# Kernel tuning notes

Hardware: AMD Instinct MI355X
Metric: run time of the kernel (lower is better)

## Reference

```python
import jax, jax.numpy as jnp
import numpy as np

N_NODES = 100000
N_EDGES = 1600000
MAX_RADIUS = 3.0
NUM_BASIS = 3
SQRT2 = 2.0 ** 0.5
# e3nn soft_one_hot_linspace 'smooth_finite' prefactor
C_SMOOTH = 1.14136 * float(np.exp(2.0))


def _sus(x):
    # smooth unit step: exp(-1/x) for x>0 else 0 (NaN-safe for grad)
    safe = jnp.where(x > 0.0, x, 1.0)
    return jnp.where(x > 0.0, jnp.exp(-1.0 / safe), 0.0)


def radial_embed(d):
    # soft_one_hot_linspace(d, 0, max_radius, 3, basis='smooth_finite', cutoff=True) * sqrt(num_basis)
    values = jnp.linspace(0.0, MAX_RADIUS, NUM_BASIS + 2)[1:-1]  # [3]
    step = MAX_RADIUS / (NUM_BASIS + 1)
    diff = (d[:, None] - values) / step  # [E,3]
    y = C_SMOOTH * _sus(diff + 1.0) * _sus(1.0 - diff)
    return y * (NUM_BASIS ** 0.5)


def fcnet(x, w1, w2):
    # e3nn FullyConnectedNet([3,16,numel], relu): normalized weights, normalize2mom(relu)=sqrt(2)*relu
    h = SQRT2 * jax.nn.relu(x @ (w1 / w1.shape[0] ** 0.5))
    return h @ (w2 / w2.shape[0] ** 0.5)


def reference(pos, feat, edge_src, edge_dst, fc1_w1, fc1_w2, core_w1, core_w2, fc3_w1, fc3_w2, conv_w, conv_b):
    n = pos.shape[0]
    z = edge_src.shape[0] / n  # average num neighbors
    edge_vec = pos[edge_dst] - pos[edge_src]
    d = jnp.sqrt(jnp.sum(edge_vec * edge_vec, axis=1))  # edges are self-loop-free -> d > 0
    emb = radial_embed(d)  # [E,3]

    # NOTE on e3nn math: with input/mid/output parities all even and sh = 0e+1o+2e,
    # the only parity-allowed paths producing nonzero output are the 0e (scalar) paths,
    # which contract against Y_0 = 1 ('component' normalization). The 4x1e block of the
    # mid irreps is identically zero (no parity-allowed path ever populates it), so the
    # math below (scalar block only, with e3nn path weights) is exactly equivalent.
    def conv(x, w1, w2, mul_in, mul_out, path_w):
        # per-edge weights from radial MLP; keep the 0e->0e instruction block
        w = fcnet(emb, w1, w2)[:, : mul_in * mul_out].reshape(-1, mul_in, mul_out)
        msg = path_w * jnp.einsum('euw,eu->ew', w, x[edge_src])
        return jax.ops.segment_sum(msg, edge_dst, num_segments=n) / z ** 0.5

    x = conv(feat, fc1_w1, fc1_w2, 3, 4, (1.0 / 3.0) ** 0.5)  # tp1: fan_in 3*1 -> pw=1/sqrt(3)
    for i in range(3):
        x = conv(x, core_w1[i], core_w2[i], 4, 4, 0.5)  # tp2 0e path: pw=sqrt(1/4)
    x = conv(x, fc3_w1, fc3_w2, 4, 16, 0.5)  # tp3: pw=sqrt(1/4)
    # Conv1d(16, 2, 1) == pointwise linear
    return x @ conv_w.T + conv_b


def setup_inputs():
    key = jax.random.key(0)
    ks = jax.random.split(key, 12)
    pos = jax.random.uniform(ks[0], (N_NODES, 3), dtype=jnp.float32)  # unit box -> all edge lengths < max_radius
    feat = jax.random.normal(ks[1], (N_NODES, 3), dtype=jnp.float32)
    edge_src = jax.random.randint(ks[2], (N_EDGES,), 0, N_NODES, dtype=jnp.int32)
    off = jax.random.randint(ks[3], (N_EDGES,), 1, N_NODES, dtype=jnp.int32)
    edge_dst = ((edge_src + off) % N_NODES).astype(jnp.int32)  # radius_graph has no self-loops
    return {
        'pos': pos,
        'feat': feat,
        'edge_src': edge_src,
        'edge_dst': edge_dst,
        'fc1_w1': jax.random.normal(ks[4], (3, 16), jnp.float32),
        'fc1_w2': jax.random.normal(ks[5], (16, 12), jnp.float32),
        'core_w1': jax.random.normal(ks[6], (3, 3, 16), jnp.float32),
        'core_w2': jax.random.normal(ks[7], (3, 16, 48), jnp.float32),
        'fc3_w1': jax.random.normal(ks[8], (3, 16), jnp.float32),
        'fc3_w2': jax.random.normal(ks[9], (16, 64), jnp.float32),
        'conv_w': jax.random.normal(ks[10], (2, 16), jnp.float32) * 0.25,
        'conv_b': jax.random.normal(ks[11], (2,), jnp.float32) * 0.1,
    }
```

## Files before the change

kernel.cpp:

```cpp
#include <hip/hip_runtime.h>


#define BCAP 4608
#define NBMAX 400

__device__ __forceinline__ float sus_f(float x) {
    return x > 0.0f ? __expf(-1.0f / x) : 0.0f;
}

__device__ __forceinline__ float uload(const float* p) {
    return __uint_as_float(__builtin_amdgcn_readfirstlane(__float_as_uint(*p)));
}

__global__ __launch_bounds__(256) void k_bin(
    const int* __restrict__ src, const int* __restrict__ dst,
    int* __restrict__ gcur, int* __restrict__ ebuf_int,
    int nedges, int nb)
{
    __shared__ int cnt[NBMAX];
    __shared__ int gb[NBMAX];
    for (int b = threadIdx.x; b < nb; b += 256) cnt[b] = 0;
    __syncthreads();
    int base = blockIdx.x * 2048;
    int pk[8]; int bk[8]; short r[8];
    #pragma unroll
    for (int i = 0; i < 8; ++i) {
        int e = base + i * 256 + threadIdx.x;
        if (e < nedges) {
            int s = src[e], t = dst[e];
            int b = t >> 8;
            bk[i] = b;
            pk[i] = (s << 8) | (t & 255);
            r[i] = (short)atomicAdd(&cnt[b], 1);
        } else bk[i] = -1;
    }
    __syncthreads();
    for (int b = threadIdx.x; b < nb; b += 256) {
        int c = cnt[b];
        gb[b] = c > 0 ? atomicAdd(&gcur[b], c) : 0;
    }
    __syncthreads();
    #pragma unroll
    for (int i = 0; i < 8; ++i) {
        if (bk[i] >= 0) {
            int p = gb[bk[i]] + (int)r[i];
            if (p < BCAP)
                ebuf_int[18432 * bk[i] + 13824 + p] = pk[i];
        }
    }
}

__global__ __launch_bounds__(256) void k_build(
    const float* __restrict__ pos, const int* __restrict__ gcur,
    float4* __restrict__ ebuf, int2* __restrict__ offs2,
    int n, int nb)
{
    int b = blockIdx.x;
    int cnt = gcur[b]; if (cnt > BCAP) cnt = BCAP;

    __shared__ int stage[BCAP];
    __shared__ unsigned short rnk[BCAP];
    __shared__ int deg[256];
    __shared__ int loffs[256];
    __shared__ float lpos[256 * 3];

    const int* tail = (const int*)ebuf + 18432 * b + 13824;
    for (int j = threadIdx.x; j < cnt; j += 256) stage[j] = tail[j];

    int nid0 = b << 8;
    int nn = n - nid0; if (nn > 256) nn = 256;
    for (int j = threadIdx.x; j < nn * 3; j += 256) lpos[j] = pos[nid0 * 3 + j];
    deg[threadIdx.x] = 0;
    __syncthreads();

    for (int j = threadIdx.x; j < cnt; j += 256) {
        int ln = stage[j] & 255;
        rnk[j] = (unsigned short)atomicAdd(&deg[ln], 1);
    }
    __syncthreads();

    {
        int t = threadIdx.x;
        int v = deg[t];
        loffs[t] = v; __syncthreads();
        for (int off = 1; off < 256; off <<= 1) {
            int val = (t >= off) ? loffs[t - off] : 0;
            __syncthreads();
            loffs[t] += val;
            __syncthreads();
        }
        int incl = loffs[t];
        __syncthreads();
        loffs[t] = incl - v;
        __syncthreads();
    }

    {
        int t = threadIdx.x;
        if (t < nn) {
            int st = b * BCAP + loffs[t];
            offs2[nid0 + t] = make_int2(st, st + deg[t]);
        }
    }

    const float C = 1.14136f * 7.3890560989306495f;
    for (int j = threadIdx.x; j < cnt; j += 256) {
        int pkd = stage[j];
        int ln = pkd & 255;
        int s = pkd >> 8;
        float dx = lpos[ln * 3 + 0] - pos[3 * s + 0];
        float dy = lpos[ln * 3 + 1] - pos[3 * s + 1];
        float dz = lpos[ln * 3 + 2] - pos[3 * s + 2];
        float d = sqrtf(dx * dx + dy * dy + dz * dz);
        float e0, e1, e2;
        { float f = (d - 0.75f) * (1.0f / 0.75f);
          e0 = C * sus_f(f + 1.0f) * sus_f(1.0f - f); }
        { float f = (d - 1.50f) * (1.0f / 0.75f);
          e1 = C * sus_f(f + 1.0f) * sus_f(1.0f - f); }
        { float f = (d - 2.25f) * (1.0f / 0.75f);
          e2 = C * sus_f(f + 1.0f) * sus_f(1.0f - f); }
        int slot = b * BCAP + loffs[ln] + (int)rnk[j];
        ebuf[slot] = make_float4(__int_as_float(s), e0, e1, e2);
    }
}


__global__ __launch_bounds__(256) void k_node_l1(
    const float* __restrict__ feat, const float4* __restrict__ edata,
    const int2* __restrict__ offs2,
    const float* __restrict__ w1, const float* __restrict__ w2,
    float* __restrict__ xout, int n)
{
    __shared__ float lw[16 * 20];
    if (threadIdx.x < 192) {
        int k = threadIdx.x / 12, r = threadIdx.x % 12;
        lw[k * 20 + r] = w2[k * 12 + r];
    }
    __syncthreads();

    int g = blockIdx.x * 256 + threadIdx.x;
    int nd = g >> 2;
    if (nd >= n) return;
    int t = g & 3;

    float w1r[3][16];
    #pragma unroll
    for (int j = 0; j < 3; ++j)
        #pragma unroll
        for (int k = 0; k < 16; ++k) w1r[j][k] = uload(&w1[j * 16 + k]);

    float O[16][3];
    #pragma unroll
    for (int k = 0; k < 16; ++k)
        #pragma unroll
        for (int u = 0; u < 3; ++u) O[k][u] = 0.0f;

    int2 se = offs2[nd];
    for (int e = se.x + t; e < se.y; e += 4) {
        float4 ed = edata[e];
        int s = __float_as_int(ed.x);
        float f0 = feat[3 * s + 0], f1 = feat[3 * s + 1], f2 = feat[3 * s + 2];
        #pragma unroll
        for (int k = 0; k < 16; ++k) {
            float a = fmaf(ed.y, w1r[0][k], fmaf(ed.z, w1r[1][k], ed.w * w1r[2][k]));
            float h = a > 0.0f ? a : 0.0f;
            O[k][0] = fmaf(h, f0, O[k][0]);
            O[k][1] = fmaf(h, f1, O[k][1]);
            O[k][2] = fmaf(h, f2, O[k][2]);
        }
    }

    float p0 = 0.f, p1 = 0.f, p2 = 0.f, p3 = 0.f;
    #pragma unroll
    for (int k = 0; k < 16; ++k)
        #pragma unroll
        for (int u = 0; u < 3; ++u) {
            const float4 q = *(const float4*)&lw[k * 20 + u * 4];
            float o = O[k][u];
            p0 = fmaf(o, q.x, p0); p1 = fmaf(o, q.y, p1);
            p2 = fmaf(o, q.z, p2); p3 = fmaf(o, q.w, p3);
        }
    p0 += __shfl_xor(p0, 1); p1 += __shfl_xor(p1, 1);
    p2 += __shfl_xor(p2, 1); p3 += __shfl_xor(p3, 1);
    p0 += __shfl_xor(p0, 2); p1 += __shfl_xor(p1, 2);
    p2 += __shfl_xor(p2, 2); p3 += __shfl_xor(p3, 2);
    if (t == 0) {
        const float S = 0.051031036307982884f;
        float4 o; o.x = p0 * S; o.y = p1 * S; o.z = p2 * S; o.w = p3 * S;
        ((float4*)xout)[nd] = o;
    }
}

__global__ __launch_bounds__(256) void k_node_core(
    const float4* __restrict__ xin, const float4* __restrict__ edata,
    const int2* __restrict__ offs2,
    const float* __restrict__ w1, const float* __restrict__ w2,
    float* __restrict__ xout, int n)
{
    __shared__ float lw[16 * 20];
    {
        int idx = threadIdx.x;
        int k = idx >> 4, r = idx & 15;
        lw[k * 20 + r] = w2[k * 48 + r];
    }
    __syncthreads();

    int g = blockIdx.x * 256 + threadIdx.x;
    int nd = g >> 2;
    if (nd >= n) return;
    int t = g & 3;

    float w1r[3][16];
    #pragma unroll
    for (int j = 0; j < 3; ++j)
        #pragma unroll
        for (int k = 0; k < 16; ++k) w1r[j][k] = uload(&w1[j * 16 + k]);

    float O[16][4];
    #pragma unroll
    for (int k = 0; k < 16; ++k)
        #pragma unroll
        for (int u = 0; u < 4; ++u) O[k][u] = 0.0f;

    int2 se = offs2[nd];
    for (int e = se.x + t; e < se.y; e += 4) {
        float4 ed = edata[e];
        int s = __float_as_int(ed.x);
        float4 x = xin[s];
        #pragma unroll
        for (int k = 0; k < 16; ++k) {
            float a = fmaf(ed.y, w1r[0][k], fmaf(ed.z, w1r[1][k], ed.w * w1r[2][k]));
            float h = a > 0.0f ? a : 0.0f;
            O[k][0] = fmaf(h, x.x, O[k][0]);
            O[k][1] = fmaf(h, x.y, O[k][1]);
            O[k][2] = fmaf(h, x.z, O[k][2]);
            O[k][3] = fmaf(h, x.w, O[k][3]);
        }
    }

    float p0 = 0.f, p1 = 0.f, p2 = 0.f, p3 = 0.f;
    #pragma unroll
    for (int k = 0; k < 16; ++k)
        #pragma unroll
        for (int u = 0; u < 4; ++u) {
            const float4 q = *(const float4*)&lw[k * 20 + u * 4];
            float o = O[k][u];
            p0 = fmaf(o, q.x, p0); p1 = fmaf(o, q.y, p1);
            p2 = fmaf(o, q.z, p2); p3 = fmaf(o, q.w, p3);
        }
    p0 += __shfl_xor(p0, 1); p1 += __shfl_xor(p1, 1);
    p2 += __shfl_xor(p2, 1); p3 += __shfl_xor(p3, 1);
    p0 += __shfl_xor(p0, 2); p1 += __shfl_xor(p1, 2);
    p2 += __shfl_xor(p2, 2); p3 += __shfl_xor(p3, 2);
    if (t == 0) {
        const float S = 0.04419417382415922f;
        float4 o; o.x = p0 * S; o.y = p1 * S; o.z = p2 * S; o.w = p3 * S;
        ((float4*)xout)[nd] = o;
    }
}

__global__ __launch_bounds__(256) void k_node_fc3_final(
    const float4* __restrict__ xin, const float4* __restrict__ edata,
    const int2* __restrict__ offs2,
    const float* __restrict__ w1, const float* __restrict__ w2,
    const float* __restrict__ cw, const float* __restrict__ cb,
    float* __restrict__ out, int n)
{
    __shared__ float lw[16 * 68];
    #pragma unroll
    for (int i = 0; i < 4; ++i) {
        int idx = threadIdx.x + i * 256;
        int k = idx >> 6, c = idx & 63;
        lw[k * 68 + c] = w2[k * 64 + c];
    }
    __syncthreads();

    int g = blockIdx.x * 256 + threadIdx.x;
    int nd = g >> 2;
    if (nd >= n) return;
    int t = g & 3;

    float w1r[3][16];
    #pragma unroll
    for (int j = 0; j < 3; ++j)
        #pragma unroll
        for (int k = 0; k < 16; ++k) w1r[j][k] = uload(&w1[j * 16 + k]);

    float O[16][4];
    #pragma unroll
    for (int k = 0; k < 16; ++k)
        #pragma unroll
        for (int u = 0; u < 4; ++u) O[k][u] = 0.0f;

    int2 se = offs2[nd];
    for (int e = se.x + t; e < se.y; e += 4) {
        float4 ed = edata[e];
        int s = __float_as_int(ed.x);
        float4 x = xin[s];
        #pragma unroll
        for (int k = 0; k < 16; ++k) {
            float a = fmaf(ed.y, w1r[0][k], fmaf(ed.z, w1r[1][k], ed.w * w1r[2][k]));
            float h = a > 0.0f ? a : 0.0f;
            O[k][0] = fmaf(h, x.x, O[k][0]);
            O[k][1] = fmaf(h, x.y, O[k][1]);
            O[k][2] = fmaf(h, x.z, O[k][2]);
            O[k][3] = fmaf(h, x.w, O[k][3]);
        }
    }

    float part[16];
    #pragma unroll
    for (int w = 0; w < 16; ++w) part[w] = 0.0f;
    #pragma unroll
    for (int k = 0; k < 16; ++k)
        #pragma unroll
        for (int u = 0; u < 4; ++u) {
            float o = O[k][u];
            const float* row = &lw[k * 68 + u * 16];
            #pragma unroll
            for (int w4 = 0; w4 < 4; ++w4) {
                const float4 q = *(const float4*)&row[w4 * 4];
                part[w4 * 4 + 0] = fmaf(o, q.x, part[w4 * 4 + 0]);
                part[w4 * 4 + 1] = fmaf(o, q.y, part[w4 * 4 + 1]);
                part[w4 * 4 + 2] = fmaf(o, q.z, part[w4 * 4 + 2]);
                part[w4 * 4 + 3] = fmaf(o, q.w, part[w4 * 4 + 3]);
            }
        }
    float a0 = 0.f, a1 = 0.f;
    #pragma unroll
    for (int w = 0; w < 16; ++w) {
        a0 = fmaf(part[w], cw[w], a0);
        a1 = fmaf(part[w], cw[16 + w], a1);
    }
    a0 += __shfl_xor(a0, 1); a1 += __shfl_xor(a1, 1);
    a0 += __shfl_xor(a0, 2); a1 += __shfl_xor(a1, 2);
    if (t == 0) {
        const float S = 0.04419417382415922f;
        float2 o; o.x = fmaf(a0, S, cb[0]); o.y = fmaf(a1, S, cb[1]);
        ((float2*)out)[nd] = o;
    }
}


extern "C" void kernel_launch(void* const* d_in, const int* in_sizes, int n_in,
                              void* d_out, int out_size, void* d_ws, size_t ws_size,
                              hipStream_t stream) {
    const float* pos     = (const float*)d_in[0];
    const float* feat    = (const float*)d_in[1];
    const int*   esrc    = (const int*)d_in[2];
    const int*   edst    = (const int*)d_in[3];
    const float* fc1_w1  = (const float*)d_in[4];
    const float* fc1_w2  = (const float*)d_in[5];
    const float* core_w1 = (const float*)d_in[6];
    const float* core_w2 = (const float*)d_in[7];
    const float* fc3_w1  = (const float*)d_in[8];
    const float* fc3_w2  = (const float*)d_in[9];
    const float* conv_w  = (const float*)d_in[10];
    const float* conv_b  = (const float*)d_in[11];
    float* out = (float*)d_out;

    const int E = in_sizes[2];
    const int N = in_sizes[0] / 3;
    const int nb = (N + 255) >> 8;

    float4* ebuf = (float4*)d_ws;
    float* xa = (float*)(ebuf + (size_t)nb * BCAP);
    float* xb = xa + (size_t)4 * N;
    int2* offs2 = (int2*)(xb + (size_t)4 * N);
    int* gcur = (int*)(offs2 + N);

    int g4 = (4 * N + 255) / 256;

    hipMemsetAsync(gcur, 0, (size_t)nb * sizeof(int), stream);
    k_bin<<<(E + 2047) / 2048, 256, 0, stream>>>(esrc, edst, gcur,
                                                 (int*)ebuf, E, nb);
    k_build<<<nb, 256, 0, stream>>>(pos, gcur, ebuf, offs2, N, nb);

    k_node_l1<<<g4, 256, 0, stream>>>(feat, ebuf, offs2, fc1_w1, fc1_w2, xa, N);
    k_node_core<<<g4, 256, 0, stream>>>((const float4*)xa, ebuf, offs2,
                                        core_w1 + 0, core_w2 + 0, xb, N);
    k_node_core<<<g4, 256, 0, stream>>>((const float4*)xb, ebuf, offs2,
                                        core_w1 + 48, core_w2 + 768, xa, N);
    k_node_core<<<g4, 256, 0, stream>>>((const float4*)xa, ebuf, offs2,
                                        core_w1 + 96, core_w2 + 1536, xb, N);
    k_node_fc3_final<<<g4, 256, 0, stream>>>((const float4*)xb, ebuf, offs2,
                                             fc3_w1, fc3_w2, conv_w, conv_b,
                                             out, N);
}
```

Before: 248.6 us.

## Compute radial embedding during binning and prefold fc3 weights with conv weights

Moves the edge-length and smooth-basis computation from k_build into k_bin, which now writes full float4 records into a separate temporary buffer instead of packed ints. k_build then only ranks and scatters the records. Separately, a tiny kernel pre-multiplies fc3_w2 by conv_w into a 128-entry table, so the final node kernel does 64 FMAs into two accumulators instead of 1024 plus a 16x2 projection. The binning change quadruples the bytes written and read through the temporary buffer and does random pos gathers for both endpoints. In exchange it removes the staging and local position loads in k_build and spreads the transcendental work across more blocks.

```diff
diff --git a/kernel.cpp b/kernel.cpp
--- a/kernel.cpp
+++ b/kernel.cpp
@@ -12,9 +12,23 @@
     return __uint_as_float(__builtin_amdgcn_readfirstlane(__float_as_uint(*p)));
 }
 
+__global__ __launch_bounds__(128) void k_prep_g(
+    const float* __restrict__ w2, const float* __restrict__ cw,
+    float* __restrict__ gbuf)
+{
+    int idx = threadIdx.x;
+    int k = idx >> 3, u = (idx >> 1) & 3, c = idx & 1;
+    float s = 0.0f;
+    #pragma unroll
+    for (int w = 0; w < 16; ++w)
+        s = fmaf(w2[k * 64 + u * 16 + w], cw[c * 16 + w], s);
+    gbuf[idx] = s;
+}
+
 __global__ __launch_bounds__(256) void k_bin(
     const int* __restrict__ src, const int* __restrict__ dst,
-    int* __restrict__ gcur, int* __restrict__ ebuf_int,
+    const float* __restrict__ pos,
+    int* __restrict__ gcur, float4* __restrict__ etmp,
     int nedges, int nb)
 {
     __shared__ int cnt[NBMAX];
@@ -40,42 +54,49 @@
         gb[b] = c > 0 ? atomicAdd(&gcur[b], c) : 0;
     }
     __syncthreads();
+    const float C = 1.14136f * 7.3890560989306495f;
     #pragma unroll
     for (int i = 0; i < 8; ++i) {
-        if (bk[i] >= 0) {
-            int p = gb[bk[i]] + (int)r[i];
-            if (p < BCAP)
-                ebuf_int[18432 * bk[i] + 13824 + p] = pk[i];
-        }
+        if (bk[i] < 0) continue;
+        int p = gb[bk[i]] + (int)r[i];
+        if (p >= BCAP) continue;
+        int s = pk[i] >> 8;
+        int t = (bk[i] << 8) | (pk[i] & 255);
+        float dx = pos[3 * t + 0] - pos[3 * s + 0];
+        float dy = pos[3 * t + 1] - pos[3 * s + 1];
+        float dz = pos[3 * t + 2] - pos[3 * s + 2];
+        float d = sqrtf(dx * dx + dy * dy + dz * dz);
+        float e0, e1, e2;
+        { float f = (d - 0.75f) * (1.0f / 0.75f);
+          e0 = C * sus_f(f + 1.0f) * sus_f(1.0f - f); }
+        { float f = (d - 1.50f) * (1.0f / 0.75f);
+          e1 = C * sus_f(f + 1.0f) * sus_f(1.0f - f); }
+        { float f = (d - 2.25f) * (1.0f / 0.75f);
+          e2 = C * sus_f(f + 1.0f) * sus_f(1.0f - f); }
+        etmp[(size_t)bk[i] * BCAP + p] =
+            make_float4(__int_as_float(pk[i]), e0, e1, e2);
     }
 }
 
 __global__ __launch_bounds__(256) void k_build(
-    const float* __restrict__ pos, const int* __restrict__ gcur,
+    const int* __restrict__ gcur, const float4* __restrict__ etmp,
     float4* __restrict__ ebuf, int2* __restrict__ offs2,
     int n, int nb)
 {
     int b = blockIdx.x;
     int cnt = gcur[b]; if (cnt > BCAP) cnt = BCAP;
 
-    __shared__ int stage[BCAP];
     __shared__ unsigned short rnk[BCAP];
     __shared__ int deg[256];
     __shared__ int loffs[256];
-    __shared__ float lpos[256 * 3];
-
-    const int* tail = (const int*)ebuf + 18432 * b + 13824;
-    for (int j = threadIdx.x; j < cnt; j += 256) stage[j] = tail[j];
-
-    int nid0 = b << 8;
-    int nn = n - nid0; if (nn > 256) nn = 256;
-    for (int j = threadIdx.x; j < nn * 3; j += 256) lpos[j] = pos[nid0 * 3 + j];
+
+    const float4* tin = etmp + (size_t)b * BCAP;
     deg[threadIdx.x] = 0;
     __syncthreads();
 
     for (int j = threadIdx.x; j < cnt; j += 256) {
-        int ln = stage[j] & 255;
-        rnk[j] = (unsigned short)atomicAdd(&deg[ln], 1);
+        int pkd = __float_as_int(tin[j].x);
+        rnk[j] = (unsigned short)atomicAdd(&deg[pkd & 255], 1);
     }
     __syncthreads();
 
@@ -96,6 +117,8 @@
     }
 
     {
+        int nid0 = b << 8;
+        int nn = n - nid0; if (nn > 256) nn = 256;
         int t = threadIdx.x;
         if (t < nn) {
             int st = b * BCAP + loffs[t];
@@ -103,24 +126,12 @@
         }
     }
 
-    const float C = 1.14136f * 7.3890560989306495f;
     for (int j = threadIdx.x; j < cnt; j += 256) {
-        int pkd = stage[j];
+        float4 rec = tin[j];
+        int pkd = __float_as_int(rec.x);
         int ln = pkd & 255;
-        int s = pkd >> 8;
-        float dx = lpos[ln * 3 + 0] - pos[3 * s + 0];
-        float dy = lpos[ln * 3 + 1] - pos[3 * s + 1];
-        float dz = lpos[ln * 3 + 2] - pos[3 * s + 2];
-        float d = sqrtf(dx * dx + dy * dy + dz * dz);
-        float e0, e1, e2;
-        { float f = (d - 0.75f) * (1.0f / 0.75f);
-          e0 = C * sus_f(f + 1.0f) * sus_f(1.0f - f); }
-        { float f = (d - 1.50f) * (1.0f / 0.75f);
-          e1 = C * sus_f(f + 1.0f) * sus_f(1.0f - f); }
-        { float f = (d - 2.25f) * (1.0f / 0.75f);
-          e2 = C * sus_f(f + 1.0f) * sus_f(1.0f - f); }
         int slot = b * BCAP + loffs[ln] + (int)rnk[j];
-        ebuf[slot] = make_float4(__int_as_float(s), e0, e1, e2);
+        ebuf[slot] = make_float4(__int_as_float(pkd >> 8), rec.y, rec.z, rec.w);
     }
 }
 
@@ -262,17 +273,12 @@
 __global__ __launch_bounds__(256) void k_node_fc3_final(
     const float4* __restrict__ xin, const float4* __restrict__ edata,
     const int2* __restrict__ offs2,
-    const float* __restrict__ w1, const float* __restrict__ w2,
-    const float* __restrict__ cw, const float* __restrict__ cb,
+    const float* __restrict__ w1, const float* __restrict__ gbuf,
+    const float* __restrict__ cb,
     float* __restrict__ out, int n)
 {
-    __shared__ float lw[16 * 68];
-    #pragma unroll
-    for (int i = 0; i < 4; ++i) {
-        int idx = threadIdx.x + i * 256;
-        int k = idx >> 6, c = idx & 63;
-        lw[k * 68 + c] = w2[k * 64 + c];
-    }
+    __shared__ float lg[128];
+    if (threadIdx.x < 128) lg[threadIdx.x] = gbuf[threadIdx.x];
     __syncthreads();
 
     int g = blockIdx.x * 256 + threadIdx.x;
@@ -308,30 +314,16 @@
         }
     }
 
-    float part[16];
-    #pragma unroll
-    for (int w = 0; w < 16; ++w) part[w] = 0.0f;
+    float a0 = 0.f, a1 = 0.f;
     #pragma unroll
     for (int k = 0; k < 16; ++k)
         #pragma unroll
         for (int u = 0; u < 4; ++u) {
             float o = O[k][u];
-            const float* row = &lw[k * 68 + u * 16];
-            #pragma unroll
-            for (int w4 = 0; w4 < 4; ++w4) {
-                const float4 q = *(const float4*)&row[w4 * 4];
-                part[w4 * 4 + 0] = fmaf(o, q.x, part[w4 * 4 + 0]);
-                part[w4 * 4 + 1] = fmaf(o, q.y, part[w4 * 4 + 1]);
-                part[w4 * 4 + 2] = fmaf(o, q.z, part[w4 * 4 + 2]);
-                part[w4 * 4 + 3] = fmaf(o, q.w, part[w4 * 4 + 3]);
-            }
-        }
-    float a0 = 0.f, a1 = 0.f;
-    #pragma unroll
-    for (int w = 0; w < 16; ++w) {
-        a0 = fmaf(part[w], cw[w], a0);
-        a1 = fmaf(part[w], cw[16 + w], a1);
-    }
+            const float2 q = *(const float2*)&lg[(k * 4 + u) * 2];
+            a0 = fmaf(o, q.x, a0);
+            a1 = fmaf(o, q.y, a1);
+        }
     a0 += __shfl_xor(a0, 1); a1 += __shfl_xor(a1, 1);
     a0 += __shfl_xor(a0, 2); a1 += __shfl_xor(a1, 2);
     if (t == 0) {
@@ -364,17 +356,20 @@
     const int nb = (N + 255) >> 8;
 
     float4* ebuf = (float4*)d_ws;
-    float* xa = (float*)(ebuf + (size_t)nb * BCAP);
+    float4* etmp = ebuf + (size_t)nb * BCAP;
+    float* xa = (float*)(etmp + (size_t)nb * BCAP);
     float* xb = xa + (size_t)4 * N;
     int2* offs2 = (int2*)(xb + (size_t)4 * N);
     int* gcur = (int*)(offs2 + N);
+    float* gbuf = (float*)(gcur + ((nb + 3) & ~3));
 
     int g4 = (4 * N + 255) / 256;
 
     hipMemsetAsync(gcur, 0, (size_t)nb * sizeof(int), stream);
-    k_bin<<<(E + 2047) / 2048, 256, 0, stream>>>(esrc, edst, gcur,
-                                                 (int*)ebuf, E, nb);
-    k_build<<<nb, 256, 0, stream>>>(pos, gcur, ebuf, offs2, N, nb);
+    k_prep_g<<<1, 128, 0, stream>>>(fc3_w2, conv_w, gbuf);
+    k_bin<<<(E + 2047) / 2048, 256, 0, stream>>>(esrc, edst, pos, gcur,
+                                                 etmp, E, nb);
+    k_build<<<nb, 256, 0, stream>>>(gcur, etmp, ebuf, offs2, N, nb);
 
     k_node_l1<<<g4, 256, 0, stream>>>(feat, ebuf, offs2, fc1_w1, fc1_w2, xa, N);
     k_node_core<<<g4, 256, 0, stream>>>((const float4*)xa, ebuf, offs2,
@@ -384,6 +379,5 @@
     k_node_core<<<g4, 256, 0, stream>>>((const float4*)xa, ebuf, offs2,
                                         core_w1 + 96, core_w2 + 1536, xb, N);
     k_node_fc3_final<<<g4, 256, 0, stream>>>((const float4*)xb, ebuf, offs2,
-                                             fc3_w1, fc3_w2, conv_w, conv_b,
-                                             out, N);
-}
+                                             fc3_w1, gbuf, conv_b, out, N);
+}
```

Result: slower. 253.7 us (+2.1%).
